# Kernel tuning notes

Measured on AMD Instinct MI355X. Metric: run time of the kernel, lower is better.

## Reference

```python
import jax, jax.numpy as jnp
import numpy as np


def setup_inputs() -> dict:
    key = jax.random.key(0)
    ks = jax.random.split(key, 5)
    B, C, H, W = 16, 512, 32, 32
    n_heads, d_k = 4, 128
    return {
        "x": jax.random.normal(ks[0], (B, C, H, W), dtype=jnp.float32),
        "w_proj": jax.random.normal(ks[1], (3 * n_heads * d_k, C), dtype=jnp.float32) * (1.0 / np.sqrt(C)),
        "b_proj": jax.random.normal(ks[2], (3 * n_heads * d_k,), dtype=jnp.float32) * 0.01,
        "w_out": jax.random.normal(ks[3], (C, n_heads * d_k), dtype=jnp.float32) * (1.0 / np.sqrt(n_heads * d_k)),
        "b_out": jax.random.normal(ks[4], (C,), dtype=jnp.float32) * 0.01,
        "n_heads": n_heads,
    }


def reference(x, w_proj, b_proj, w_out, b_out, n_heads):
    B, C, H, W = x.shape
    seq = H * W
    d_k = (w_proj.shape[0] // 3) // n_heads
    scale = d_k ** -0.5

    xs = x.reshape(B, C, seq).transpose(0, 2, 1)          # [B, seq, C]
    qkv = xs @ w_proj.T + b_proj                           # [B, seq, 3*H*d_k]
    qkv = qkv.reshape(B, seq, n_heads, 3 * d_k)
    q, k, v = jnp.split(qkv, 3, axis=-1)                   # each [B, seq, H, d_k]

    attn = jnp.einsum('bihd,bjhd->bijh', q, k) * scale     # [B, seq, seq, H]
    # NOTE: softmax over the QUERY axis (dim=1), faithful to the source quirk.
    attn = jax.nn.softmax(attn, axis=1)

    res = jnp.einsum('bijh,bjhd->bihd', attn, v)           # [B, seq, H, d_k]
    res = res.reshape(B, seq, n_heads * d_k)
    res = res @ w_out.T + b_out + xs                       # residual add
    return res.transpose(0, 2, 1).reshape(B, C, H, W)
```

## Files before the change

### kernel.cpp

```cpp
#include <hip/hip_runtime.h>
#include <hip/hip_bf16.h>
#include <math.h>

#define B_    16
#define CIN   512
#define SEQ   1024
#define NH    4
#define DK    128
#define OUT3  1536
#define SCALE 0.08838834764831845f
#define CSHIFT 8.0f

typedef __attribute__((ext_vector_type(8))) __bf16 bf16x8;
typedef __attribute__((ext_vector_type(4))) float f32x4;

#define MFMA(a, b, c) __builtin_amdgcn_mfma_f32_16x16x32_bf16((a), (b), (c), 0, 0, 0)

__device__ __forceinline__ ushort f2bf(float f) {
    __hip_bfloat16 h = __float2bfloat16(f);
    return *(ushort*)&h;
}
__device__ __forceinline__ uint pk2(float a, float b) {
    return (uint)f2bf(a) | ((uint)f2bf(b) << 16);
}
__device__ __forceinline__ void g2l16(const ushort* g, ushort* l) {
    __builtin_amdgcn_global_load_lds(
        (const __attribute__((address_space(1))) unsigned int*)g,
        (__attribute__((address_space(3))) unsigned int*)l, 16, 0, 0);
}
__device__ __forceinline__ int xcdswz(int bid, int nwg) {
    return (bid & 7) * (nwg >> 3) + (bid >> 3);
}

__global__ __launch_bounds__(256) void transpose_cast_kernel(
    const float* __restrict__ x, ushort* __restrict__ xt)
{
    __shared__ ushort t[64 * 66];
    const int tid = threadIdx.x;
    const int i0 = blockIdx.x * 64, c0 = blockIdx.y * 64, b = blockIdx.z;

    #pragma unroll
    for (int l = 0; l < 4; ++l) {
        int idx = tid + l * 256;
        int c = idx >> 4, i4 = (idx & 15) << 2;
        float4 v = *(const float4*)&x[((size_t)b * CIN + c0 + c) * SEQ + i0 + i4];
        t[(i4 + 0) * 66 + c] = f2bf(v.x);
        t[(i4 + 1) * 66 + c] = f2bf(v.y);
        t[(i4 + 2) * 66 + c] = f2bf(v.z);
        t[(i4 + 3) * 66 + c] = f2bf(v.w);
    }
    __syncthreads();
    #pragma unroll
    for (int l = 0; l < 4; ++l) {
        int idx = tid + l * 256;
        int i = idx >> 4, c4 = (idx & 15) << 2;
        uint2 p;
        p.x = *(const uint*)&t[i * 66 + c4];
        p.y = *(const uint*)&t[i * 66 + c4 + 2];
        *(uint2*)&xt[((size_t)b * SEQ + i0 + i) * CIN + c0 + c4] = p;
    }
}

__global__ __launch_bounds__(256) void cast_kernel(
    const float* __restrict__ src, ushort* __restrict__ dst, int n4)
{
    int idx = blockIdx.x * 256 + threadIdx.x;
    if (idx < n4) {
        float4 v = *(const float4*)&src[(size_t)idx * 4];
        uint2 p; p.x = pk2(v.x, v.y); p.y = pk2(v.z, v.w);
        *(uint2*)&dst[(size_t)idx * 4] = p;
    }
}

__global__ __launch_bounds__(256) void qkv_kernel(
    const ushort* __restrict__ wbf, const float* __restrict__ bias,
    const ushort* __restrict__ xt,
    ushort* __restrict__ qb, ushort* __restrict__ kb, ushort* __restrict__ vtb)
{
    __shared__ __attribute__((aligned(16))) ushort lds_a0[128 * 32];
    __shared__ __attribute__((aligned(16))) ushort lds_a1[128 * 32];
    __shared__ __attribute__((aligned(16))) ushort lds_b0[128 * 32];
    __shared__ __attribute__((aligned(16))) ushort lds_b1[128 * 32];
    const int tid = threadIdx.x;
    const int lane = tid & 63, wv = tid >> 6;
    const int l15 = lane & 15, l4 = lane >> 4;
    const int wm = wv >> 1, wn = wv & 1;
    const int swz = xcdswz(blockIdx.x, 1536);
    const int o0 = (swz % 12) * 128;
    const int i0 = ((swz / 12) & 7) * 128;
    const int b  = swz / 96;

    auto stage = [&](int c0, ushort* la, ushort* lb) {
        #pragma unroll
        for (int l = 0; l < 2; ++l) {
            int chunk = l * 256 + tid;
            int row = chunk >> 2, c = chunk & 3;
            g2l16(&wbf[(size_t)(o0 + row) * CIN + c0 + (c << 3)],
                  &la[(size_t)(l * 256 + wv * 64) * 8]);
        }
        #pragma unroll
        for (int l = 0; l < 2; ++l) {
            int chunk = l * 256 + tid;
            int row = chunk >> 2, c = chunk & 3;
            g2l16(&xt[((size_t)b * SEQ + i0 + row) * CIN + c0 + (c << 3)],
                  &lb[(size_t)(l * 256 + wv * 64) * 8]);
        }
    };

    f32x4 acc[4][4] = {};
    stage(0, lds_a0, lds_b0);
    __syncthreads();
    for (int it = 0; it < CIN / 32; ++it) {
        const ushort* la = (it & 1) ? lds_a1 : lds_a0;
        const ushort* lb = (it & 1) ? lds_b1 : lds_b0;
        if (it + 1 < CIN / 32)
            stage((it + 1) * 32, (it & 1) ? lds_a0 : lds_a1,
                                 (it & 1) ? lds_b0 : lds_b1);
        bf16x8 af[4], bfv[4];
        #pragma unroll
        for (int m = 0; m < 4; ++m)
            af[m] = *(const bf16x8*)&la[(wm * 64 + m * 16 + l15) * 32 + (l4 << 3)];
        #pragma unroll
        for (int n = 0; n < 4; ++n)
            bfv[n] = *(const bf16x8*)&lb[(wn * 64 + n * 16 + l15) * 32 + (l4 << 3)];
        #pragma unroll
        for (int m = 0; m < 4; ++m)
            #pragma unroll
            for (int n = 0; n < 4; ++n)
                acc[m][n] = MFMA(af[m], bfv[n], acc[m][n]);
        __syncthreads();
    }
    const int h = o0 / 384, which = (o0 % 384) / 128;
    const int bh = b * NH + h;
    #pragma unroll
    for (int m = 0; m < 4; ++m) {
        const int d0 = wm * 64 + m * 16 + (l4 << 2);
        float bia[4];
        #pragma unroll
        for (int r = 0; r < 4; ++r) bia[r] = bias[o0 + d0 + r];
        #pragma unroll
        for (int n = 0; n < 4; ++n) {
            const int i = i0 + wn * 64 + n * 16 + l15;
            float v0 = acc[m][n][0] + bia[0], v1 = acc[m][n][1] + bia[1];
            float v2 = acc[m][n][2] + bia[2], v3 = acc[m][n][3] + bia[3];
            if (which == 2) {
                vtb[((size_t)bh * DK + d0 + 0) * SEQ + i] = f2bf(v0);
                vtb[((size_t)bh * DK + d0 + 1) * SEQ + i] = f2bf(v1);
                vtb[((size_t)bh * DK + d0 + 2) * SEQ + i] = f2bf(v2);
                vtb[((size_t)bh * DK + d0 + 3) * SEQ + i] = f2bf(v3);
            } else {
                ushort* dst = (which == 0) ? qb : kb;
                uint2 p; p.x = pk2(v0, v1); p.y = pk2(v2, v3);
                *(uint2*)&dst[((size_t)bh * SEQ + i) * DK + d0] = p;
            }
        }
    }
}

__global__ __launch_bounds__(256) void stats_kernel(
    const ushort* __restrict__ qb, const ushort* __restrict__ kb,
    float* __restrict__ cstat)
{
    __shared__ __attribute__((aligned(16))) ushort lds_q0[64 * 128];
    __shared__ __attribute__((aligned(16))) ushort lds_q1[64 * 128];
    const int tid = threadIdx.x;
    const int lane = tid & 63, wv = tid >> 6;
    const int l15 = lane & 15, l4 = lane >> 4;
    const int swz = xcdswz(blockIdx.x, 512);
    const int bh = swz >> 3;
    const int j0 = (swz & 7) * 128 + wv * 32;
    const ushort* kbase = kb + (size_t)bh * SEQ * DK;
    const ushort* qbase = qb + (size_t)bh * SEQ * DK;

    auto stageQ = [&](int it, ushort* dst) {
        #pragma unroll
        for (int l = 0; l < 4; ++l) {
            int chunk = l * 256 + tid;
            int row = chunk >> 4, c = chunk & 15;
            g2l16(&qbase[(size_t)(it * 64 + row) * DK + ((c ^ (row & 7)) << 3)],
                  &dst[(size_t)(l * 256 + wv * 64) * 8]);
        }
    };

    bf16x8 kf[2][4];
    #pragma unroll
    for (int m = 0; m < 2; ++m)
        #pragma unroll
        for (int ks = 0; ks < 4; ++ks)
            kf[m][ks] = *(const bf16x8*)&kbase[(size_t)(j0 + m * 16 + l15) * DK
                                               + ks * 32 + (l4 << 3)];
    float ss[2][4] = {};

    stageQ(0, lds_q0);
    __syncthreads();
    for (int it = 0; it < SEQ / 64; ++it) {
        const ushort* lq = (it & 1) ? lds_q1 : lds_q0;
        if (it + 1 < SEQ / 64)
            stageQ(it + 1, (it & 1) ? lds_q0 : lds_q1);
        f32x4 sa0[4], sa1[4];
        __builtin_amdgcn_s_setprio(1);
        #pragma unroll
        for (int n = 0; n < 4; ++n) {
            f32x4 a0 = {}, a1 = {};
            #pragma unroll
            for (int ks = 0; ks < 4; ++ks) {
                bf16x8 bq = *(const bf16x8*)&lq[(n * 16 + l15) * 128
                                + ((((ks << 2) | l4) ^ (l15 & 7)) << 3)];
                a0 = MFMA(kf[0][ks], bq, a0);
                a1 = MFMA(kf[1][ks], bq, a1);
            }
            sa0[n] = a0; sa1[n] = a1;
        }
        __builtin_amdgcn_s_setprio(0);
        #pragma unroll
        for (int r = 0; r < 4; ++r) {
            float e0 = 0.0f, e1 = 0.0f;
            #pragma unroll
            for (int n = 0; n < 4; ++n) {
                e0 += __expf(fmaf(sa0[n][r], SCALE, -CSHIFT));
                e1 += __expf(fmaf(sa1[n][r], SCALE, -CSHIFT));
            }
            ss[0][r] += e0;
            ss[1][r] += e1;
        }
        __syncthreads();
    }
    #pragma unroll
    for (int m = 0; m < 2; ++m)
        #pragma unroll
        for (int r = 0; r < 4; ++r) {
            float sv = ss[m][r];
            #pragma unroll
            for (int wmask = 1; wmask < 16; wmask <<= 1)
                sv += __shfl_xor(sv, wmask, 64);
            if (l15 == 0) {
                int j = j0 + m * 16 + (l4 << 2) + r;
                cstat[(size_t)bh * SEQ + j] = CSHIFT + __logf(sv);
            }
        }
}

__global__ __launch_bounds__(256) void attn_kernel(
    const ushort* __restrict__ qb, const ushort* __restrict__ kb,
    const ushort* __restrict__ vtb, const float* __restrict__ cstat,
    ushort* __restrict__ resb)
{
    __shared__ __attribute__((aligned(16))) ushort lds_k[64 * 128];
    __shared__ __attribute__((aligned(16))) ushort lds_vt[128 * 64];
    __shared__ __attribute__((aligned(16))) ushort lds_p[64 * 64];
    const int tid = threadIdx.x;
    const int lane = tid & 63, wv = tid >> 6;
    const int l15 = lane & 15, l4 = lane >> 4;
    const int wj = wv & 1, wi = wv >> 1;
    const int swz = xcdswz(blockIdx.x, 1024);
    const int bh = swz >> 4, b = bh >> 2, h = bh & 3;
    const int i0 = (swz & 15) * 64;
    const ushort* qbase = qb + (size_t)bh * SEQ * DK;
    const ushort* kbase = kb + (size_t)bh * SEQ * DK;
    const ushort* vtbase = vtb + (size_t)bh * DK * SEQ;
    const float* cbase = cstat + (size_t)bh * SEQ;

    auto stageK = [&](int j0t) {
        #pragma unroll
        for (int l = 0; l < 4; ++l) {
            int chunk = l * 256 + tid;
            int row = chunk >> 4, c = chunk & 15;
            g2l16(&kbase[(size_t)(j0t + row) * DK + ((c ^ (row & 7)) << 3)],
                  &lds_k[(size_t)(l * 256 + wv * 64) * 8]);
        }
    };
    auto stageVt = [&](int j0t) {
        #pragma unroll
        for (int l = 0; l < 4; ++l) {
            int chunk = l * 256 + tid;
            int row = chunk >> 3, c = chunk & 7;
            g2l16(&vtbase[(size_t)row * SEQ + j0t + ((c ^ (row & 7)) << 3)],
                  &lds_vt[(size_t)(l * 256 + wv * 64) * 8]);
        }
    };

    bf16x8 qf[2][4];
    #pragma unroll
    for (int n = 0; n < 2; ++n)
        #pragma unroll
        for (int ks = 0; ks < 4; ++ks)
            qf[n][ks] = *(const bf16x8*)&qbase[(size_t)(i0 + wi * 32 + n * 16 + l15) * DK
                                               + ks * 32 + (l4 << 3)];
    f32x4 oacc[2][4] = {};

    stageK(0);
    __syncthreads();
    for (int jt = 0; jt < SEQ / 64; ++jt) {
        const int j0 = jt * 64;
        stageVt(j0);
        float4 cs0 = *(const float4*)&cbase[j0 + wj * 32 + (l4 << 2)];
        float4 cs1 = *(const float4*)&cbase[j0 + wj * 32 + 16 + (l4 << 2)];
        float nc[2][4] = {{-cs0.x, -cs0.y, -cs0.z, -cs0.w},
                          {-cs1.x, -cs1.y, -cs1.z, -cs1.w}};
        bf16x8 af[2][4];
        #pragma unroll
        for (int m = 0; m < 2; ++m)
            #pragma unroll
            for (int ks = 0; ks < 4; ++ks)
                af[m][ks] = *(const bf16x8*)&lds_k[(wj * 32 + m * 16 + l15) * 128
                                + ((((ks << 2) | l4) ^ (l15 & 7)) << 3)];
        __builtin_amdgcn_s_setprio(1);
        #pragma unroll
        for (int m = 0; m < 2; ++m)
            #pragma unroll
            for (int n = 0; n < 2; ++n) {
                f32x4 s = {};
                #pragma unroll
                for (int ks = 0; ks < 4; ++ks)
                    s = MFMA(af[m][ks], qf[n][ks], s);
                const int i = wi * 32 + n * 16 + l15;
                float p0 = __expf(fmaf(s[0], SCALE, nc[m][0]));
                float p1 = __expf(fmaf(s[1], SCALE, nc[m][1]));
                float p2 = __expf(fmaf(s[2], SCALE, nc[m][2]));
                float p3 = __expf(fmaf(s[3], SCALE, nc[m][3]));
                uint2 pp; pp.x = pk2(p0, p1); pp.y = pk2(p2, p3);
                const int c8 = wj * 4 + m * 2 + (l4 >> 1);
                *(uint2*)((char*)lds_p + i * 128
                          + ((c8 ^ (i & 7)) << 4) + ((l4 & 1) << 3)) = pp;
            }
        __builtin_amdgcn_s_setprio(0);
        __syncthreads();
        if (jt + 1 < SEQ / 64) stageK(j0 + 64);
        __builtin_amdgcn_s_setprio(1);
        #pragma unroll
        for (int ks = 0; ks < 2; ++ks) {
            bf16x8 va0 = *(const bf16x8*)&lds_vt[(wv * 32 + l15) * 64
                            + ((((ks << 2) | l4) ^ (l15 & 7)) << 3)];
            bf16x8 va1 = *(const bf16x8*)&lds_vt[(wv * 32 + 16 + l15) * 64
                            + ((((ks << 2) | l4) ^ (l15 & 7)) << 3)];
            #pragma unroll
            for (int n = 0; n < 4; ++n) {
                const int row = n * 16 + l15;
                const int c8 = ks * 4 + l4;
                bf16x8 pb = *(const bf16x8*)((const char*)lds_p + row * 128
                                + ((c8 ^ (row & 7)) << 4));
                oacc[0][n] = MFMA(va0, pb, oacc[0][n]);
                oacc[1][n] = MFMA(va1, pb, oacc[1][n]);
            }
        }
        __builtin_amdgcn_s_setprio(0);
        __syncthreads();
    }
    #pragma unroll
    for (int m = 0; m < 2; ++m)
        #pragma unroll
        for (int n = 0; n < 4; ++n) {
            const int i = i0 + n * 16 + l15;
            const int d = wv * 32 + m * 16 + (l4 << 2);
            uint2 p;
            p.x = pk2(oacc[m][n][0], oacc[m][n][1]);
            p.y = pk2(oacc[m][n][2], oacc[m][n][3]);
            *(uint2*)&resb[((size_t)b * SEQ + i) * (NH * DK) + h * DK + d] = p;
        }
}

__global__ __launch_bounds__(256) void outproj_kernel(
    const ushort* __restrict__ resb, const ushort* __restrict__ woutbf,
    const float* __restrict__ bout, const float* __restrict__ x,
    float* __restrict__ out)
{
    __shared__ __attribute__((aligned(16))) ushort lds_a0[128 * 32];
    __shared__ __attribute__((aligned(16))) ushort lds_a1[128 * 32];
    __shared__ __attribute__((aligned(16))) ushort lds_b0[128 * 32];
    __shared__ __attribute__((aligned(16))) ushort lds_b1[128 * 32];
    const int tid = threadIdx.x;
    const int lane = tid & 63, wv = tid >> 6;
    const int l15 = lane & 15, l4 = lane >> 4;
    const int wm = wv >> 1, wn = wv & 1;
    const int swz = xcdswz(blockIdx.x, 512);
    const int i0 = (swz & 7) * 128;
    const int c0 = ((swz >> 3) & 3) * 128;
    const int b  = swz >> 5;

    auto stage = [&](int k0, ushort* la, ushort* lb) {
        #pragma unroll
        for (int l = 0; l < 2; ++l) {
            int chunk = l * 256 + tid;
            int row = chunk >> 2, c = chunk & 3;
            g2l16(&woutbf[(size_t)(c0 + row) * (NH * DK) + k0 + (c << 3)],
                  &la[(size_t)(l * 256 + wv * 64) * 8]);
        }
        #pragma unroll
        for (int l = 0; l < 2; ++l) {
            int chunk = l * 256 + tid;
            int row = chunk >> 2, c = chunk & 3;
            g2l16(&resb[((size_t)b * SEQ + i0 + row) * (NH * DK) + k0 + (c << 3)],
                  &lb[(size_t)(l * 256 + wv * 64) * 8]);
        }
    };

    f32x4 acc[4][4] = {};
    stage(0, lds_a0, lds_b0);
    __syncthreads();
    for (int it = 0; it < (NH * DK) / 32; ++it) {
        const ushort* la = (it & 1) ? lds_a1 : lds_a0;
        const ushort* lb = (it & 1) ? lds_b1 : lds_b0;
        if (it + 1 < (NH * DK) / 32)
            stage((it + 1) * 32, (it & 1) ? lds_a0 : lds_a1,
                                 (it & 1) ? lds_b0 : lds_b1);
        bf16x8 af[4], bfv[4];
        #pragma unroll
        for (int m = 0; m < 4; ++m)
            af[m] = *(const bf16x8*)&la[(wm * 64 + m * 16 + l15) * 32 + (l4 << 3)];
        #pragma unroll
        for (int n = 0; n < 4; ++n)
            bfv[n] = *(const bf16x8*)&lb[(wn * 64 + n * 16 + l15) * 32 + (l4 << 3)];
        #pragma unroll
        for (int m = 0; m < 4; ++m)
            #pragma unroll
            for (int n = 0; n < 4; ++n)
                acc[m][n] = MFMA(af[m], bfv[n], acc[m][n]);
        __syncthreads();
    }
    #pragma unroll
    for (int m = 0; m < 4; ++m) {
        const int cb = c0 + wm * 64 + m * 16 + (l4 << 2);
        float bia[4];
        #pragma unroll
        for (int r = 0; r < 4; ++r) bia[r] = bout[cb + r];
        #pragma unroll
        for (int n = 0; n < 4; ++n) {
            const int i = i0 + wn * 64 + n * 16 + l15;
            #pragma unroll
            for (int r = 0; r < 4; ++r) {
                size_t off = ((size_t)b * CIN + cb + r) * SEQ + i;
                out[off] = acc[m][n][r] + bia[r] + x[off];
            }
        }
    }
}

extern "C" void kernel_launch(void* const* d_in, const int* in_sizes, int n_in,
                              void* d_out, int out_size, void* d_ws, size_t ws_size,
                              hipStream_t stream) {
    const float* x      = (const float*)d_in[0];
    const float* w_proj = (const float*)d_in[1];
    const float* b_proj = (const float*)d_in[2];
    const float* w_out  = (const float*)d_in[3];
    const float* b_out  = (const float*)d_in[4];

    const size_t xtE = (size_t)B_ * SEQ * CIN;
    const size_t qkE = (size_t)B_ * NH * SEQ * DK;
    ushort* xt    = (ushort*)d_ws;
    ushort* qb    = xt + xtE;
    ushort* kb    = qb + qkE;
    ushort* vtb   = kb + qkE;
    float*  cstat = (float*)(vtb + qkE);
    ushort* resb  = (ushort*)(cstat + 2 * (size_t)B_ * NH * SEQ);
    ushort* wobf  = resb + (size_t)B_ * SEQ * (NH * DK);
    ushort* wpbf  = resb;
    float*  out   = (float*)d_out;

    transpose_cast_kernel<<<dim3(SEQ / 64, CIN / 64, B_), 256, 0, stream>>>(x, xt);
    cast_kernel<<<dim3(768), 256, 0, stream>>>(w_proj, wpbf, 196608);
    cast_kernel<<<dim3(256), 256, 0, stream>>>(w_out, wobf, 65536);
    qkv_kernel<<<dim3(1536), 256, 0, stream>>>(wpbf, b_proj, xt, qb, kb, vtb);
    stats_kernel<<<dim3(512), 256, 0, stream>>>(qb, kb, cstat);
    attn_kernel<<<dim3(1024), 256, 0, stream>>>(qb, kb, vtb, cstat, resb);
    outproj_kernel<<<dim3(512), 256, 0, stream>>>(resb, wobf, b_out, x, out);
}
```

Baseline: 239.2 us.

## Double-buffer K/V/stat tiles in attention with vmcnt-based pipelining, exp2 math

Restructures the attention inner loop into a double-buffered pipeline: K, V^T and column stats are staged into alternating LDS buffers with async global-to-LDS loads, and waits use explicit vmcnt counts instead of full barriers after each load. Column stats now come through LDS rather than per-thread global loads. Exponentials switch to exp2 with log2e folded into the scale and shift constants (stats stored in log2 domain). The two weight cast launches are merged into one kernel. This raises LDS usage, which may lower occupancy, and hand-tuned vmcnt values are fragile.

```diff
diff --git a/kernel.cpp b/kernel.cpp
--- a/kernel.cpp
+++ b/kernel.cpp
@@ -8,8 +8,10 @@
 #define NH    4
 #define DK    128
 #define OUT3  1536
+#define NT    16
 #define SCALE 0.08838834764831845f
-#define CSHIFT 8.0f
+#define SCALE_L2E  0.12751743360f
+#define CSHIFT_L2E 11.54156032711f
 
 typedef __attribute__((ext_vector_type(8))) __bf16 bf16x8;
 typedef __attribute__((ext_vector_type(4))) float f32x4;
@@ -62,13 +64,19 @@
 }
 
 __global__ __launch_bounds__(256) void cast_kernel(
-    const float* __restrict__ src, ushort* __restrict__ dst, int n4)
+    const float* __restrict__ wp, const float* __restrict__ wo,
+    ushort* __restrict__ dwp, ushort* __restrict__ dwo)
 {
     int idx = blockIdx.x * 256 + threadIdx.x;
-    if (idx < n4) {
-        float4 v = *(const float4*)&src[(size_t)idx * 4];
+    if (idx < 196608) {
+        float4 v = *(const float4*)&wp[(size_t)idx * 4];
         uint2 p; p.x = pk2(v.x, v.y); p.y = pk2(v.z, v.w);
-        *(uint2*)&dst[(size_t)idx * 4] = p;
+        *(uint2*)&dwp[(size_t)idx * 4] = p;
+    } else {
+        int j = idx - 196608;
+        float4 v = *(const float4*)&wo[(size_t)j * 4];
+        uint2 p; p.x = pk2(v.x, v.y); p.y = pk2(v.z, v.w);
+        *(uint2*)&dwo[(size_t)j * 4] = p;
     }
 }
 
@@ -217,8 +225,8 @@
             float e0 = 0.0f, e1 = 0.0f;
             #pragma unroll
             for (int n = 0; n < 4; ++n) {
-                e0 += __expf(fmaf(sa0[n][r], SCALE, -CSHIFT));
-                e1 += __expf(fmaf(sa1[n][r], SCALE, -CSHIFT));
+                e0 += exp2f(fmaf(sa0[n][r], SCALE_L2E, -CSHIFT_L2E));
+                e1 += exp2f(fmaf(sa1[n][r], SCALE_L2E, -CSHIFT_L2E));
             }
             ss[0][r] += e0;
             ss[1][r] += e1;
@@ -235,7 +243,7 @@
                 sv += __shfl_xor(sv, wmask, 64);
             if (l15 == 0) {
                 int j = j0 + m * 16 + (l4 << 2) + r;
-                cstat[(size_t)bh * SEQ + j] = CSHIFT + __logf(sv);
+                cstat[(size_t)bh * SEQ + j] = CSHIFT_L2E + __log2f(sv);
             }
         }
 }
@@ -245,9 +253,10 @@
     const ushort* __restrict__ vtb, const float* __restrict__ cstat,
     ushort* __restrict__ resb)
 {
-    __shared__ __attribute__((aligned(16))) ushort lds_k[64 * 128];
-    __shared__ __attribute__((aligned(16))) ushort lds_vt[128 * 64];
-    __shared__ __attribute__((aligned(16))) ushort lds_p[64 * 64];
+    __shared__ __attribute__((aligned(16))) ushort K0[64 * 128], K1[64 * 128];
+    __shared__ __attribute__((aligned(16))) ushort V0[128 * 64], V1[128 * 64];
+    __shared__ __attribute__((aligned(16))) ushort P[64 * 64];
+    __shared__ __attribute__((aligned(16))) float  C0[64], C1[64];
     const int tid = threadIdx.x;
     const int lane = tid & 63, wv = tid >> 6;
     const int l15 = lane & 15, l4 = lane >> 4;
@@ -260,23 +269,30 @@
     const ushort* vtbase = vtb + (size_t)bh * DK * SEQ;
     const float* cbase = cstat + (size_t)bh * SEQ;
 
-    auto stageK = [&](int j0t) {
+    auto stageK = [&](ushort* dst, int jt) {
+        const int j0t = jt * 64;
         #pragma unroll
         for (int l = 0; l < 4; ++l) {
             int chunk = l * 256 + tid;
             int row = chunk >> 4, c = chunk & 15;
             g2l16(&kbase[(size_t)(j0t + row) * DK + ((c ^ (row & 7)) << 3)],
-                  &lds_k[(size_t)(l * 256 + wv * 64) * 8]);
-        }
-    };
-    auto stageVt = [&](int j0t) {
+                  &dst[(size_t)(l * 256 + wv * 64) * 8]);
+        }
+    };
+    auto stageVt = [&](ushort* dst, int jt) {
+        const int j0t = jt * 64;
         #pragma unroll
         for (int l = 0; l < 4; ++l) {
             int chunk = l * 256 + tid;
             int row = chunk >> 3, c = chunk & 7;
             g2l16(&vtbase[(size_t)row * SEQ + j0t + ((c ^ (row & 7)) << 3)],
-                  &lds_vt[(size_t)(l * 256 + wv * 64) * 8]);
-        }
+                  &dst[(size_t)(l * 256 + wv * 64) * 8]);
+        }
+    };
+    auto stageC = [&](float* dst, int jt) {
+        __builtin_amdgcn_global_load_lds(
+            (const __attribute__((address_space(1))) unsigned int*)(cbase + jt * 64 + lane),
+            (__attribute__((address_space(3))) unsigned int*)dst, 4, 0, 0);
     };
 
     bf16x8 qf[2][4];
@@ -288,13 +304,9 @@
                                                + ks * 32 + (l4 << 3)];
     f32x4 oacc[2][4] = {};
 
-    stageK(0);
-    __syncthreads();
-    for (int jt = 0; jt < SEQ / 64; ++jt) {
-        const int j0 = jt * 64;
-        stageVt(j0);
-        float4 cs0 = *(const float4*)&cbase[j0 + wj * 32 + (l4 << 2)];
-        float4 cs1 = *(const float4*)&cbase[j0 + wj * 32 + 16 + (l4 << 2)];
+    auto phaseA = [&](int jt, const ushort* Krd, const float* Crd) {
+        float4 cs0 = *(const float4*)&Crd[wj * 32 + (l4 << 2)];
+        float4 cs1 = *(const float4*)&Crd[wj * 32 + 16 + (l4 << 2)];
         float nc[2][4] = {{-cs0.x, -cs0.y, -cs0.z, -cs0.w},
                           {-cs1.x, -cs1.y, -cs1.z, -cs1.w}};
         bf16x8 af[2][4];
@@ -302,7 +314,7 @@
         for (int m = 0; m < 2; ++m)
             #pragma unroll
             for (int ks = 0; ks < 4; ++ks)
-                af[m][ks] = *(const bf16x8*)&lds_k[(wj * 32 + m * 16 + l15) * 128
+                af[m][ks] = *(const bf16x8*)&Krd[(wj * 32 + m * 16 + l15) * 128
                                 + ((((ks << 2) | l4) ^ (l15 & 7)) << 3)];
         __builtin_amdgcn_s_setprio(1);
         #pragma unroll
@@ -314,38 +326,65 @@
                 for (int ks = 0; ks < 4; ++ks)
                     s = MFMA(af[m][ks], qf[n][ks], s);
                 const int i = wi * 32 + n * 16 + l15;
-                float p0 = __expf(fmaf(s[0], SCALE, nc[m][0]));
-                float p1 = __expf(fmaf(s[1], SCALE, nc[m][1]));
-                float p2 = __expf(fmaf(s[2], SCALE, nc[m][2]));
-                float p3 = __expf(fmaf(s[3], SCALE, nc[m][3]));
+                float p0 = exp2f(fmaf(s[0], SCALE_L2E, nc[m][0]));
+                float p1 = exp2f(fmaf(s[1], SCALE_L2E, nc[m][1]));
+                float p2 = exp2f(fmaf(s[2], SCALE_L2E, nc[m][2]));
+                float p3 = exp2f(fmaf(s[3], SCALE_L2E, nc[m][3]));
                 uint2 pp; pp.x = pk2(p0, p1); pp.y = pk2(p2, p3);
                 const int c8 = wj * 4 + m * 2 + (l4 >> 1);
-                *(uint2*)((char*)lds_p + i * 128
+                *(uint2*)((char*)P + i * 128
                           + ((c8 ^ (i & 7)) << 4) + ((l4 & 1) << 3)) = pp;
             }
         __builtin_amdgcn_s_setprio(0);
-        __syncthreads();
-        if (jt + 1 < SEQ / 64) stageK(j0 + 64);
+    };
+    auto phaseB = [&](const ushort* Vrd) {
         __builtin_amdgcn_s_setprio(1);
         #pragma unroll
         for (int ks = 0; ks < 2; ++ks) {
-            bf16x8 va0 = *(const bf16x8*)&lds_vt[(wv * 32 + l15) * 64
+            bf16x8 va0 = *(const bf16x8*)&Vrd[(wv * 32 + l15) * 64
                             + ((((ks << 2) | l4) ^ (l15 & 7)) << 3)];
-            bf16x8 va1 = *(const bf16x8*)&lds_vt[(wv * 32 + 16 + l15) * 64
+            bf16x8 va1 = *(const bf16x8*)&Vrd[(wv * 32 + 16 + l15) * 64
                             + ((((ks << 2) | l4) ^ (l15 & 7)) << 3)];
             #pragma unroll
             for (int n = 0; n < 4; ++n) {
                 const int row = n * 16 + l15;
                 const int c8 = ks * 4 + l4;
-                bf16x8 pb = *(const bf16x8*)((const char*)lds_p + row * 128
+                bf16x8 pb = *(const bf16x8*)((const char*)P + row * 128
                                 + ((c8 ^ (row & 7)) << 4));
                 oacc[0][n] = MFMA(va0, pb, oacc[0][n]);
                 oacc[1][n] = MFMA(va1, pb, oacc[1][n]);
             }
         }
         __builtin_amdgcn_s_setprio(0);
-        __syncthreads();
-    }
+    };
+
+    auto tile = [&](int t, const ushort* Krd, const float* Crd, const ushort* Vrd,
+                    ushort* Vwr, ushort* Kwr, float* Cwr, int mode) {
+        if (mode < 2) asm volatile("s_waitcnt vmcnt(9)" ::: "memory");
+        else          asm volatile("s_waitcnt vmcnt(4)" ::: "memory");
+        __builtin_amdgcn_s_barrier();
+        __builtin_amdgcn_sched_barrier(0);
+        if (mode < 2) stageVt(Vwr, t + 1);
+        phaseA(t, Krd, Crd);
+        if (mode < 2) asm volatile("s_waitcnt vmcnt(9) lgkmcnt(0)" ::: "memory");
+        else          asm volatile("s_waitcnt vmcnt(0) lgkmcnt(0)" ::: "memory");
+        __builtin_amdgcn_s_barrier();
+        __builtin_amdgcn_sched_barrier(0);
+        if (mode == 0) { stageK(Kwr, t + 2); stageC(Cwr, t + 2); }
+        phaseB(Vrd);
+    };
+
+    stageK(K0, 0); stageC(C0, 0);
+    stageK(K1, 1); stageC(C1, 1);
+    stageVt(V0, 0);
+
+    for (int t = 0; t < NT - 2; t += 2) {
+        tile(t,     K0, C0, V0, V1, K0, C0, 0);
+        tile(t + 1, K1, C1, V1, V0, K1, C1, 0);
+    }
+    tile(NT - 2, K0, C0, V0, V1, K0, C0, 1);
+    tile(NT - 1, K1, C1, V1, V0, K0, C0, 2);
+
     #pragma unroll
     for (int m = 0; m < 2; ++m)
         #pragma unroll
@@ -457,8 +496,7 @@
     float*  out   = (float*)d_out;
 
     transpose_cast_kernel<<<dim3(SEQ / 64, CIN / 64, B_), 256, 0, stream>>>(x, xt);
-    cast_kernel<<<dim3(768), 256, 0, stream>>>(w_proj, wpbf, 196608);
-    cast_kernel<<<dim3(256), 256, 0, stream>>>(w_out, wobf, 65536);
+    cast_kernel<<<dim3(1024), 256, 0, stream>>>(w_proj, w_out, wpbf, wobf);
     qkv_kernel<<<dim3(1536), 256, 0, stream>>>(wpbf, b_proj, xt, qb, kb, vtb);
     stats_kernel<<<dim3(512), 256, 0, stream>>>(qb, kb, cstat);
     attn_kernel<<<dim3(1024), 256, 0, stream>>>(qb, kb, vtb, cstat, resb);
```

New measurement: 244.3 us. +2.1%, slower.

## Enlarge attention query tile to 128, use exp2 softmax, merge weight cast launches

Applied to the files above, without the earlier changes.

The attention kernel now handles 128 queries per block instead of 64, halving the grid and reusing each staged K/Vt tile for twice as many queries. The P buffer in shared memory and the accumulators grow to match. Exponentials switch to exp2f with a log2e-prescaled scale and shift, which removes a multiply inside exp. The two weight-cast launches are merged into one kernel. The larger tile raises register and LDS use, which may lower occupancy, and 512 blocks may underfill the GPU.

```diff
diff --git a/kernel.cpp b/kernel.cpp
--- a/kernel.cpp
+++ b/kernel.cpp
@@ -8,8 +8,10 @@
 #define NH    4
 #define DK    128
 #define OUT3  1536
+#define NT    16
 #define SCALE 0.08838834764831845f
-#define CSHIFT 8.0f
+#define SCALE_L2E  0.12751743360f
+#define CSHIFT_L2E 11.54156032711f
 
 typedef __attribute__((ext_vector_type(8))) __bf16 bf16x8;
 typedef __attribute__((ext_vector_type(4))) float f32x4;
@@ -62,13 +64,19 @@
 }
 
 __global__ __launch_bounds__(256) void cast_kernel(
-    const float* __restrict__ src, ushort* __restrict__ dst, int n4)
+    const float* __restrict__ wp, const float* __restrict__ wo,
+    ushort* __restrict__ dwp, ushort* __restrict__ dwo)
 {
     int idx = blockIdx.x * 256 + threadIdx.x;
-    if (idx < n4) {
-        float4 v = *(const float4*)&src[(size_t)idx * 4];
+    if (idx < 196608) {
+        float4 v = *(const float4*)&wp[(size_t)idx * 4];
         uint2 p; p.x = pk2(v.x, v.y); p.y = pk2(v.z, v.w);
-        *(uint2*)&dst[(size_t)idx * 4] = p;
+        *(uint2*)&dwp[(size_t)idx * 4] = p;
+    } else {
+        int j = idx - 196608;
+        float4 v = *(const float4*)&wo[(size_t)j * 4];
+        uint2 p; p.x = pk2(v.x, v.y); p.y = pk2(v.z, v.w);
+        *(uint2*)&dwo[(size_t)j * 4] = p;
     }
 }
 
@@ -217,8 +225,8 @@
             float e0 = 0.0f, e1 = 0.0f;
             #pragma unroll
             for (int n = 0; n < 4; ++n) {
-                e0 += __expf(fmaf(sa0[n][r], SCALE, -CSHIFT));
-                e1 += __expf(fmaf(sa1[n][r], SCALE, -CSHIFT));
+                e0 += exp2f(fmaf(sa0[n][r], SCALE_L2E, -CSHIFT_L2E));
+                e1 += exp2f(fmaf(sa1[n][r], SCALE_L2E, -CSHIFT_L2E));
             }
             ss[0][r] += e0;
             ss[1][r] += e1;
@@ -235,7 +243,7 @@
                 sv += __shfl_xor(sv, wmask, 64);
             if (l15 == 0) {
                 int j = j0 + m * 16 + (l4 << 2) + r;
-                cstat[(size_t)bh * SEQ + j] = CSHIFT + __logf(sv);
+                cstat[(size_t)bh * SEQ + j] = CSHIFT_L2E + __log2f(sv);
             }
         }
 }
@@ -247,14 +255,14 @@
 {
     __shared__ __attribute__((aligned(16))) ushort lds_k[64 * 128];
     __shared__ __attribute__((aligned(16))) ushort lds_vt[128 * 64];
-    __shared__ __attribute__((aligned(16))) ushort lds_p[64 * 64];
+    __shared__ __attribute__((aligned(16))) ushort lds_p[128 * 64];
     const int tid = threadIdx.x;
     const int lane = tid & 63, wv = tid >> 6;
     const int l15 = lane & 15, l4 = lane >> 4;
     const int wj = wv & 1, wi = wv >> 1;
-    const int swz = xcdswz(blockIdx.x, 1024);
-    const int bh = swz >> 4, b = bh >> 2, h = bh & 3;
-    const int i0 = (swz & 15) * 64;
+    const int swz = xcdswz(blockIdx.x, 512);
+    const int bh = swz >> 3, b = bh >> 2, h = bh & 3;
+    const int i0 = (swz & 7) * 128;
     const ushort* qbase = qb + (size_t)bh * SEQ * DK;
     const ushort* kbase = kb + (size_t)bh * SEQ * DK;
     const ushort* vtbase = vtb + (size_t)bh * DK * SEQ;
@@ -279,18 +287,18 @@
         }
     };
 
-    bf16x8 qf[2][4];
-    #pragma unroll
-    for (int n = 0; n < 2; ++n)
+    bf16x8 qf[4][4];
+    #pragma unroll
+    for (int n = 0; n < 4; ++n)
         #pragma unroll
         for (int ks = 0; ks < 4; ++ks)
-            qf[n][ks] = *(const bf16x8*)&qbase[(size_t)(i0 + wi * 32 + n * 16 + l15) * DK
+            qf[n][ks] = *(const bf16x8*)&qbase[(size_t)(i0 + wi * 64 + n * 16 + l15) * DK
                                                + ks * 32 + (l4 << 3)];
-    f32x4 oacc[2][4] = {};
+    f32x4 oacc[2][8] = {};
 
     stageK(0);
     __syncthreads();
-    for (int jt = 0; jt < SEQ / 64; ++jt) {
+    for (int jt = 0; jt < NT; ++jt) {
         const int j0 = jt * 64;
         stageVt(j0);
         float4 cs0 = *(const float4*)&cbase[j0 + wj * 32 + (l4 << 2)];
@@ -308,16 +316,16 @@
         #pragma unroll
         for (int m = 0; m < 2; ++m)
             #pragma unroll
-            for (int n = 0; n < 2; ++n) {
+            for (int n = 0; n < 4; ++n) {
                 f32x4 s = {};
                 #pragma unroll
                 for (int ks = 0; ks < 4; ++ks)
                     s = MFMA(af[m][ks], qf[n][ks], s);
-                const int i = wi * 32 + n * 16 + l15;
-                float p0 = __expf(fmaf(s[0], SCALE, nc[m][0]));
-                float p1 = __expf(fmaf(s[1], SCALE, nc[m][1]));
-                float p2 = __expf(fmaf(s[2], SCALE, nc[m][2]));
-                float p3 = __expf(fmaf(s[3], SCALE, nc[m][3]));
+                const int i = wi * 64 + n * 16 + l15;
+                float p0 = exp2f(fmaf(s[0], SCALE_L2E, nc[m][0]));
+                float p1 = exp2f(fmaf(s[1], SCALE_L2E, nc[m][1]));
+                float p2 = exp2f(fmaf(s[2], SCALE_L2E, nc[m][2]));
+                float p3 = exp2f(fmaf(s[3], SCALE_L2E, nc[m][3]));
                 uint2 pp; pp.x = pk2(p0, p1); pp.y = pk2(p2, p3);
                 const int c8 = wj * 4 + m * 2 + (l4 >> 1);
                 *(uint2*)((char*)lds_p + i * 128
@@ -325,7 +333,7 @@
             }
         __builtin_amdgcn_s_setprio(0);
         __syncthreads();
-        if (jt + 1 < SEQ / 64) stageK(j0 + 64);
+        if (jt + 1 < NT) stageK(j0 + 64);
         __builtin_amdgcn_s_setprio(1);
         #pragma unroll
         for (int ks = 0; ks < 2; ++ks) {
@@ -334,7 +342,7 @@
             bf16x8 va1 = *(const bf16x8*)&lds_vt[(wv * 32 + 16 + l15) * 64
                             + ((((ks << 2) | l4) ^ (l15 & 7)) << 3)];
             #pragma unroll
-            for (int n = 0; n < 4; ++n) {
+            for (int n = 0; n < 8; ++n) {
                 const int row = n * 16 + l15;
                 const int c8 = ks * 4 + l4;
                 bf16x8 pb = *(const bf16x8*)((const char*)lds_p + row * 128
@@ -349,7 +357,7 @@
     #pragma unroll
     for (int m = 0; m < 2; ++m)
         #pragma unroll
-        for (int n = 0; n < 4; ++n) {
+        for (int n = 0; n < 8; ++n) {
             const int i = i0 + n * 16 + l15;
             const int d = wv * 32 + m * 16 + (l4 << 2);
             uint2 p;
@@ -457,10 +465,9 @@
     float*  out   = (float*)d_out;
 
     transpose_cast_kernel<<<dim3(SEQ / 64, CIN / 64, B_), 256, 0, stream>>>(x, xt);
-    cast_kernel<<<dim3(768), 256, 0, stream>>>(w_proj, wpbf, 196608);
-    cast_kernel<<<dim3(256), 256, 0, stream>>>(w_out, wobf, 65536);
+    cast_kernel<<<dim3(1024), 256, 0, stream>>>(w_proj, w_out, wpbf, wobf);
     qkv_kernel<<<dim3(1536), 256, 0, stream>>>(wpbf, b_proj, xt, qb, kb, vtb);
     stats_kernel<<<dim3(512), 256, 0, stream>>>(qb, kb, cstat);
-    attn_kernel<<<dim3(1024), 256, 0, stream>>>(qb, kb, vtb, cstat, resb);
+    attn_kernel<<<dim3(512), 256, 0, stream>>>(qb, kb, vtb, cstat, resb);
     outproj_kernel<<<dim3(512), 256, 0, stream>>>(resb, wobf, b_out, x, out);
 }
```

After: 241.1 us. Within noise of the previous version (+0.8%).
